# Optimization experiments

Measured on AMD Instinct MI355X. Metric: run time of the kernel, lower is better.

The kernel has to match this reference:

```python
import jax, jax.numpy as jnp
import numpy as np

B, T, C = 4, 2048, 1024
H = 16
D = C // H  # head_dim = 64

def setup_inputs() -> dict:
    key = jax.random.key(0)
    k1, k2, k3 = jax.random.split(key, 3)
    x = jax.random.normal(k1, (B, T, C), dtype=jnp.float32)
    Wqkv = jax.random.normal(k2, (C, 3 * C), dtype=jnp.float32) * (C ** -0.5)
    Wproj = jax.random.normal(k3, (C, C), dtype=jnp.float32) * (C ** -0.5)
    return {"x": x, "Wqkv": Wqkv, "Wproj": Wproj}

def reference(x, Wqkv, Wproj):
    b, t, c = x.shape
    qkv = (x @ Wqkv).reshape(b, t, 3, H, D)
    qkv = jnp.transpose(qkv, (2, 0, 3, 1, 4))  # [3, B, H, T, D]
    q, k, v = qkv[0], qkv[1], qkv[2]
    att = jnp.einsum('bhqd,bhkd->bhqk', q, k) * (D ** -0.5)
    causal = jnp.tril(jnp.ones((t, t), dtype=bool))  # True where allowed
    att = jnp.where(causal, att, -jnp.inf)
    att = jax.nn.softmax(att, axis=-1)
    out = jnp.einsum('bhqk,bhkd->bhqd', att, v)  # [B, H, T, D]
    out = jnp.transpose(out, (0, 2, 1, 3)).reshape(b, t, c)
    return out @ Wproj
```

## Files before the change

### kernel.cpp

```cpp
#include <hip/hip_runtime.h>
#include <stdint.h>

typedef unsigned short u16;
typedef __bf16 bf16x8 __attribute__((ext_vector_type(8)));
typedef float f32x4 __attribute__((ext_vector_type(4)));

#define DEVI static __device__ __forceinline__

DEVI u16 f2bf(float f) {
  union { float f; unsigned u; } v; v.f = f;
  unsigned r = v.u + 0x7FFF + ((v.u >> 16) & 1);
  return (u16)(r >> 16);
}

DEVI unsigned pkbf(float a, float b) {
  union { float f; unsigned u; } x, y; x.f = a; y.f = b;
  return __builtin_amdgcn_perm(y.u + 0x8000u, x.u + 0x8000u, 0x07060302u);
}

DEVI void lds_fence() { asm volatile("s_waitcnt lgkmcnt(0)" ::: "memory"); }

DEVI void gl2lds16(const u16* g, u16* l) {
  __builtin_amdgcn_global_load_lds(
      (const __attribute__((address_space(1))) unsigned int*)(uintptr_t)g,
      (__attribute__((address_space(3))) unsigned int*)(uintptr_t)l,
      16, 0, 0);
}

__global__ __launch_bounds__(256)
void prep(const float* __restrict__ x, u16* __restrict__ xb,
          const float* __restrict__ Wqkv, u16* __restrict__ wqkvT,
          const float* __restrict__ Wproj, u16* __restrict__ wprojT) {
  __shared__ float tile[64][65];
  const int blk = blockIdx.x;
  if (blk < 8192) {
    const int i = blk * 256 + threadIdx.x;
    const float4 v = ((const float4*)x)[i];
    ushort4 o;
    o.x = f2bf(v.x); o.y = f2bf(v.y); o.z = f2bf(v.z); o.w = f2bf(v.w);
    ((ushort4*)xb)[i] = o;
    return;
  }
  const float* in; u16* out; int Cn, n0, r0;
  if (blk < 8960) {
    const int p = blk - 8192;
    in = Wqkv; out = wqkvT; Cn = 3072;
    n0 = (p % 48) * 64; r0 = (p / 48) * 64;
  } else {
    const int p = blk - 8960;
    in = Wproj; out = wprojT; Cn = 1024;
    n0 = (p % 16) * 64; r0 = (p / 16) * 64;
  }
#pragma unroll
  for (int i = 0; i < 16; ++i) {
    const int e = threadIdx.x + i * 256;
    const int r = e >> 6, c = e & 63;
    tile[r][c] = in[(size_t)(r0 + r) * Cn + n0 + c];
  }
  __syncthreads();
#pragma unroll
  for (int i = 0; i < 16; ++i) {
    const int e = threadIdx.x + i * 256;
    const int r = e >> 6, c = e & 63;
    out[(size_t)(n0 + r) * 1024 + r0 + c] = f2bf(tile[c][r]);
  }
}

template <int MODE>
__global__ __launch_bounds__(256)
void gemm128(const u16* __restrict__ A, const u16* __restrict__ Bt,
             int M, int N, int K, float* __restrict__ Cout,
             u16* __restrict__ Qg, u16* __restrict__ Kg, u16* __restrict__ Vtg) {
  __shared__ alignas(16) u16 As0[128 * 32];
  __shared__ alignas(16) u16 As1[128 * 32];
  __shared__ alignas(16) u16 Bs0[128 * 32];
  __shared__ alignas(16) u16 Bs1[128 * 32];
  const int tid = threadIdx.x;
  const int wave = tid >> 6, lane = tid & 63;
  const int quad = lane >> 4, l15 = lane & 15;
  const int m0 = blockIdx.y * 128;
  const int n0 = blockIdx.x * 128;
  const int wm = (wave >> 1) * 64;
  const int wn = (wave & 1) * 64;

  f32x4 acc[4][4] = {};

  const int q1 = wave * 64 + lane;
  const int q2 = q1 + 256;
  const int r1 = q1 >> 2, c1 = q1 & 3;
  const int r2 = q2 >> 2, c2 = q2 & 3;
  const size_t ga1 = (size_t)(m0 + r1) * K + c1 * 8;
  const size_t ga2 = (size_t)(m0 + r2) * K + c2 * 8;
  const size_t gb1 = (size_t)(n0 + r1) * K + c1 * 8;
  const size_t gb2 = (size_t)(n0 + r2) * K + c2 * 8;

  for (int k0 = 0; k0 < K; k0 += 64) {
    __syncthreads();
    gl2lds16(A + ga1 + k0, As0 + wave * 512);
    gl2lds16(A + ga2 + k0, As0 + 2048 + wave * 512);
    gl2lds16(Bt + gb1 + k0, Bs0 + wave * 512);
    gl2lds16(Bt + gb2 + k0, Bs0 + 2048 + wave * 512);
    gl2lds16(A + ga1 + k0 + 32, As1 + wave * 512);
    gl2lds16(A + ga2 + k0 + 32, As1 + 2048 + wave * 512);
    gl2lds16(Bt + gb1 + k0 + 32, Bs1 + wave * 512);
    gl2lds16(Bt + gb2 + k0 + 32, Bs1 + 2048 + wave * 512);
    __syncthreads();
#pragma unroll
    for (int kh = 0; kh < 2; ++kh) {
      const u16* Asl = kh ? As1 : As0;
      const u16* Bsl = kh ? Bs1 : Bs0;
      bf16x8 av[4], bv[4];
#pragma unroll
      for (int i = 0; i < 4; ++i)
        av[i] = *(const bf16x8*)(Asl + (wm + i * 16 + l15) * 32 + quad * 8);
#pragma unroll
      for (int j = 0; j < 4; ++j)
        bv[j] = *(const bf16x8*)(Bsl + (wn + j * 16 + l15) * 32 + quad * 8);
#pragma unroll
      for (int i = 0; i < 4; ++i)
#pragma unroll
        for (int j = 0; j < 4; ++j)
          acc[i][j] = __builtin_amdgcn_mfma_f32_16x16x32_bf16(av[i], bv[j], acc[i][j], 0, 0, 0);
    }
  }

  if constexpr (MODE == 0) {
#pragma unroll
    for (int i = 0; i < 4; ++i) {
#pragma unroll
      for (int j = 0; j < 4; ++j) {
        const int mb = m0 + wm + i * 16 + quad * 4;
        const int n = n0 + wn + j * 16 + l15;
#pragma unroll
        for (int r = 0; r < 4; ++r)
          Cout[(size_t)(mb + r) * N + n] = acc[i][j][r];
      }
    }
  } else {
    const int s0b = n0 >> 10;
    const int b = m0 >> 11;
    const int h = ((n0 + wn) >> 6) & 15;
    const int bh = b * 16 + h;
    const int tbase = (m0 & 2047) + wm;
    if (s0b == 2) {
      __syncthreads();
      u16* sl = (wave < 2 ? As0 : Bs0) + (wave & 1) * 2048;
#pragma unroll
      for (int jp = 0; jp < 2; ++jp) {
#pragma unroll
        for (int j2 = 0; j2 < 2; ++j2) {
          const int j = jp * 2 + j2;
          const int dl = j2 * 16 + l15;
          const int sw8 = dl & 7;
#pragma unroll
          for (int i = 0; i < 4; ++i) {
            const int tq = i * 2 + (quad >> 1);
            ushort4 pk;
            pk.x = f2bf(acc[i][j][0]); pk.y = f2bf(acc[i][j][1]);
            pk.z = f2bf(acc[i][j][2]); pk.w = f2bf(acc[i][j][3]);
            *(ushort4*)(sl + dl * 64 + ((tq ^ sw8) << 3) + (quad & 1) * 4) = pk;
          }
        }
        lds_fence();
#pragma unroll
        for (int p = 0; p < 4; ++p) {
          const int dl = p * 8 + (lane >> 3);
          const int tc = lane & 7;
          const int tcu = tc ^ (dl & 7);
          const uint4 v = *(const uint4*)(sl + dl * 64 + tc * 8);
          *(uint4*)(Vtg + ((size_t)(bh * 64 + jp * 32 + dl)) * 2048 + tbase + tcu * 8) = v;
        }
        lds_fence();
      }
    } else {
      u16* dst = s0b ? Kg : Qg;
      const float scale = s0b ? 1.0f : 0.18033688f;
#pragma unroll
      for (int i = 0; i < 4; ++i) {
        const int t0 = tbase + i * 16 + quad * 4;
#pragma unroll
        for (int j = 0; j < 4; ++j) {
          const int d = j * 16 + l15;
#pragma unroll
          for (int r = 0; r < 4; ++r)
            dst[((size_t)bh * 2048 + t0 + r) * 64 + d] = f2bf(acc[i][j][r] * scale);
        }
      }
    }
  }
}

__global__ __launch_bounds__(256)
void attn_fwd(const u16* __restrict__ Qg, const u16* __restrict__ Kg,
              const u16* __restrict__ Vtg, u16* __restrict__ Og) {
  __shared__ alignas(16) u16 Ks[2][64 * 64];
  __shared__ alignas(16) u16 Vts[2][64 * 64];
  __shared__ alignas(16) u16 Ps[4][16 * 64];

  const int tid = threadIdx.x;
  const int wave = tid >> 6, lane = tid & 63;
  const int quad = lane >> 4, l15 = lane & 15;
  const int bh = blockIdx.x & 63;
  const int qt = 15 - (blockIdx.x >> 6);
  const int b = bh >> 4, h = bh & 15;
  const int sw = l15 & 7;

  const int rs0 = wave * 16 + (lane >> 3);
  const int rs1 = rs0 + 8;
  const int cs = (lane & 7) ^ (rs0 & 7);
  const size_t kgb0 = (size_t)(bh * 2048 + rs0) * 64 + cs * 8;
  const size_t kgb1 = (size_t)(bh * 2048 + rs1) * 64 + cs * 8;
  const size_t vgb0 = (size_t)(bh * 64 + rs0) * 2048 + cs * 8;
  const size_t vgb1 = (size_t)(bh * 64 + rs1) * 2048 + cs * 8;
  const int ldsw0 = wave * 1024;
  const int ldsw1 = wave * 1024 + 512;

  const int qb0 = qt * 128 + wave * 32;

  bf16x8 bq[2][2];
#pragma unroll
  for (int qs = 0; qs < 2; ++qs)
#pragma unroll
    for (int hv = 0; hv < 2; ++hv)
      bq[qs][hv] = *(const bf16x8*)(Qg + ((size_t)bh * 2048 + qb0 + qs * 16 + l15) * 64 + hv * 32 + quad * 8);

  f32x4 oacc[2][4] = {};
  float li[2] = {0.f, 0.f};

  const int jlast = qt * 128 + 64;
  const int nt = (jlast >> 6) + 1;

  gl2lds16(Kg + kgb0, Ks[0] + ldsw0);
  gl2lds16(Kg + kgb1, Ks[0] + ldsw1);
  gl2lds16(Vtg + vgb0, Vts[0] + ldsw0);
  gl2lds16(Vtg + vgb1, Vts[0] + ldsw1);
  asm volatile("s_waitcnt vmcnt(0)" ::: "memory");
  __builtin_amdgcn_s_barrier();

  for (int t = 0; t < nt; ++t) {
    const int j0 = t << 6;
    const int cur = t & 1;
    if (t + 1 < nt) {
      const size_t ko = (size_t)(j0 + 64) * 64;
      gl2lds16(Kg + kgb0 + ko, Ks[cur ^ 1] + ldsw0);
      gl2lds16(Kg + kgb1 + ko, Ks[cur ^ 1] + ldsw1);
      gl2lds16(Vtg + vgb0 + j0 + 64, Vts[cur ^ 1] + ldsw0);
      gl2lds16(Vtg + vgb1 + j0 + 64, Vts[cur ^ 1] + ldsw1);
    }

    if (j0 <= qb0 + 31) {
      __builtin_amdgcn_s_setprio(1);
      const u16* Kc = Ks[cur];
      const u16* Vc = Vts[cur];
      bf16x8 aK[4][2];
#pragma unroll
      for (int ks = 0; ks < 4; ++ks)
#pragma unroll
        for (int hv = 0; hv < 2; ++hv)
          aK[ks][hv] = *(const bf16x8*)(Kc + (ks * 16 + l15) * 64 + ((hv * 4 + quad) ^ sw) * 8);
      bf16x8 bV[4][2];
#pragma unroll
      for (int ds = 0; ds < 4; ++ds)
#pragma unroll
        for (int kc = 0; kc < 2; ++kc)
          bV[ds][kc] = *(const bf16x8*)(Vc + (ds * 16 + l15) * 64 + ((kc * 4 + quad) ^ sw) * 8);

#pragma unroll
      for (int qs = 0; qs < 2; ++qs) {
        const int qb = qb0 + qs * 16;
        if (j0 > qb + 15) continue;
        u16* Pw = Ps[wave];
        const bool needmask = (j0 + 63 > qb);
#pragma unroll
        for (int ks = 0; ks < 4; ++ks) {
          f32x4 s = {};
          s = __builtin_amdgcn_mfma_f32_16x16x32_bf16(aK[ks][0], bq[qs][0], s, 0, 0, 0);
          s = __builtin_amdgcn_mfma_f32_16x16x32_bf16(aK[ks][1], bq[qs][1], s, 0, 0, 0);
          if (needmask) {
            const int kbase = j0 + ks * 16 + quad * 4;
            const int qrow = qb + l15;
#pragma unroll
            for (int r = 0; r < 4; ++r)
              if (kbase + r > qrow) s[r] = -1e30f;
          }
          float p0 = __builtin_amdgcn_exp2f(s[0]);
          float p1 = __builtin_amdgcn_exp2f(s[1]);
          float p2 = __builtin_amdgcn_exp2f(s[2]);
          float p3 = __builtin_amdgcn_exp2f(s[3]);
          li[qs] += (p0 + p1) + (p2 + p3);
          uint2 pk;
          pk.x = pkbf(p0, p1);
          pk.y = pkbf(p2, p3);
          *(uint2*)(Pw + l15 * 64 + (((ks * 2 + (quad >> 1)) ^ sw) * 8) + (quad & 1) * 4) = pk;
        }
        lds_fence();
        bf16x8 aP0 = *(const bf16x8*)(Pw + l15 * 64 + ((0 * 4 + quad) ^ sw) * 8);
        bf16x8 aP1 = *(const bf16x8*)(Pw + l15 * 64 + ((1 * 4 + quad) ^ sw) * 8);
#pragma unroll
        for (int ds = 0; ds < 4; ++ds) {
          oacc[qs][ds] = __builtin_amdgcn_mfma_f32_16x16x32_bf16(aP0, bV[ds][0], oacc[qs][ds], 0, 0, 0);
          oacc[qs][ds] = __builtin_amdgcn_mfma_f32_16x16x32_bf16(aP1, bV[ds][1], oacc[qs][ds], 0, 0, 0);
        }
      }
      __builtin_amdgcn_s_setprio(0);
    }

    asm volatile("s_waitcnt vmcnt(0)" ::: "memory");
    __builtin_amdgcn_s_barrier();
  }

#pragma unroll
  for (int qs = 0; qs < 2; ++qs) {
    float l = li[qs];
    l += __shfl_xor(l, 16);
    l += __shfl_xor(l, 32);
    const int qb = qb0 + qs * 16;
#pragma unroll
    for (int r = 0; r < 4; ++r) {
      const float lrow = __shfl(l, quad * 4 + r);
      const float inv = 1.0f / lrow;
      u16* orow = Og + ((size_t)b * 2048 + qb + quad * 4 + r) * 1024 + h * 64;
#pragma unroll
      for (int ds = 0; ds < 4; ++ds)
        orow[ds * 16 + l15] = f2bf(oacc[qs][ds][r] * inv);
    }
  }
}

extern "C" void kernel_launch(void* const* d_in, const int* in_sizes, int n_in,
                              void* d_out, int out_size, void* d_ws, size_t ws_size,
                              hipStream_t stream) {
  const float* x = (const float*)d_in[0];
  const float* Wqkv = (const float*)d_in[1];
  const float* Wproj = (const float*)d_in[2];
  float* out = (float*)d_out;

  char* ws = (char*)d_ws;
  u16* xb     = (u16*)(ws);
  u16* wqkvT  = (u16*)(ws + 16777216);
  u16* wprojT = (u16*)(ws + 23068672);
  u16* Qg     = (u16*)(ws + 25165824);
  u16* Kg     = (u16*)(ws + 41943040);
  u16* Vtg    = (u16*)(ws + 58720256);
  u16* Og     = (u16*)(ws + 75497472);

  prep<<<9216, 256, 0, stream>>>(x, xb, Wqkv, wqkvT, Wproj, wprojT);
  gemm128<1><<<dim3(24, 64), 256, 0, stream>>>(xb, wqkvT, 8192, 3072, 1024,
                                               nullptr, Qg, Kg, Vtg);
  attn_fwd<<<1024, 256, 0, stream>>>(Qg, Kg, Vtg, Og);
  gemm128<0><<<dim3(8, 64), 256, 0, stream>>>(Og, wprojT, 8192, 1024, 1024,
                                              out, nullptr, nullptr, nullptr);
}
```

Before: 243.3 us.

## Pair complementary 64-row query tiles per block for causal load balance

```diff
diff --git a/kernel.cpp b/kernel.cpp
--- a/kernel.cpp
+++ b/kernel.cpp
@@ -201,7 +201,7 @@
   const int wave = tid >> 6, lane = tid & 63;
   const int quad = lane >> 4, l15 = lane & 15;
   const int bh = blockIdx.x & 63;
-  const int qt = 15 - (blockIdx.x >> 6);
+  const int ip = blockIdx.x >> 6;
   const int b = bh >> 4, h = bh & 15;
   const int sw = l15 & 7;
 
@@ -215,40 +215,35 @@
   const int ldsw0 = wave * 1024;
   const int ldsw1 = wave * 1024 + 512;
 
-  const int qb0 = qt * 128 + wave * 32;
-
-  bf16x8 bq[2][2];
-#pragma unroll
-  for (int qs = 0; qs < 2; ++qs)
-#pragma unroll
-    for (int hv = 0; hv < 2; ++hv)
-      bq[qs][hv] = *(const bf16x8*)(Qg + ((size_t)bh * 2048 + qb0 + qs * 16 + l15) * 64 + hv * 32 + quad * 8);
-
-  f32x4 oacc[2][4] = {};
-  float li[2] = {0.f, 0.f};
-
-  const int jlast = qt * 128 + 64;
-  const int nt = (jlast >> 6) + 1;
-
-  gl2lds16(Kg + kgb0, Ks[0] + ldsw0);
-  gl2lds16(Kg + kgb1, Ks[0] + ldsw1);
-  gl2lds16(Vtg + vgb0, Vts[0] + ldsw0);
-  gl2lds16(Vtg + vgb1, Vts[0] + ldsw1);
-  asm volatile("s_waitcnt vmcnt(0)" ::: "memory");
-  __builtin_amdgcn_s_barrier();
-
-  for (int t = 0; t < nt; ++t) {
-    const int j0 = t << 6;
-    const int cur = t & 1;
-    if (t + 1 < nt) {
-      const size_t ko = (size_t)(j0 + 64) * 64;
-      gl2lds16(Kg + kgb0 + ko, Ks[cur ^ 1] + ldsw0);
-      gl2lds16(Kg + kgb1 + ko, Ks[cur ^ 1] + ldsw1);
-      gl2lds16(Vtg + vgb0 + j0 + 64, Vts[cur ^ 1] + ldsw0);
-      gl2lds16(Vtg + vgb1 + j0 + 64, Vts[cur ^ 1] + ldsw1);
-    }
-
-    if (j0 <= qb0 + 31) {
+#pragma unroll 1
+  for (int ph = 0; ph < 2; ++ph) {
+    const int g = ph ? ip : (31 - ip);
+    const int qb = g * 64 + wave * 16;
+
+    const bf16x8 bq0 = *(const bf16x8*)(Qg + ((size_t)bh * 2048 + qb + l15) * 64 + quad * 8);
+    const bf16x8 bq1 = *(const bf16x8*)(Qg + ((size_t)bh * 2048 + qb + l15) * 64 + 32 + quad * 8);
+
+    f32x4 oacc[4] = {};
+    float li = 0.f;
+
+    gl2lds16(Kg + kgb0, Ks[0] + ldsw0);
+    gl2lds16(Kg + kgb1, Ks[0] + ldsw1);
+    gl2lds16(Vtg + vgb0, Vts[0] + ldsw0);
+    gl2lds16(Vtg + vgb1, Vts[0] + ldsw1);
+    asm volatile("s_waitcnt vmcnt(0)" ::: "memory");
+    __builtin_amdgcn_s_barrier();
+
+    for (int t = 0; t <= g; ++t) {
+      const int j0 = t << 6;
+      const int cur = t & 1;
+      if (t < g) {
+        const size_t ko = (size_t)(j0 + 64) * 64;
+        gl2lds16(Kg + kgb0 + ko, Ks[cur ^ 1] + ldsw0);
+        gl2lds16(Kg + kgb1 + ko, Ks[cur ^ 1] + ldsw1);
+        gl2lds16(Vtg + vgb0 + j0 + 64, Vts[cur ^ 1] + ldsw0);
+        gl2lds16(Vtg + vgb1 + j0 + 64, Vts[cur ^ 1] + ldsw1);
+      }
+
       __builtin_amdgcn_s_setprio(1);
       const u16* Kc = Ks[cur];
       const u16* Vc = Vts[cur];
@@ -265,56 +260,47 @@
         for (int kc = 0; kc < 2; ++kc)
           bV[ds][kc] = *(const bf16x8*)(Vc + (ds * 16 + l15) * 64 + ((kc * 4 + quad) ^ sw) * 8);
 
-#pragma unroll
-      for (int qs = 0; qs < 2; ++qs) {
-        const int qb = qb0 + qs * 16;
-        if (j0 > qb + 15) continue;
-        u16* Pw = Ps[wave];
-        const bool needmask = (j0 + 63 > qb);
-#pragma unroll
-        for (int ks = 0; ks < 4; ++ks) {
-          f32x4 s = {};
-          s = __builtin_amdgcn_mfma_f32_16x16x32_bf16(aK[ks][0], bq[qs][0], s, 0, 0, 0);
-          s = __builtin_amdgcn_mfma_f32_16x16x32_bf16(aK[ks][1], bq[qs][1], s, 0, 0, 0);
-          if (needmask) {
-            const int kbase = j0 + ks * 16 + quad * 4;
-            const int qrow = qb + l15;
-#pragma unroll
-            for (int r = 0; r < 4; ++r)
-              if (kbase + r > qrow) s[r] = -1e30f;
-          }
-          float p0 = __builtin_amdgcn_exp2f(s[0]);
-          float p1 = __builtin_amdgcn_exp2f(s[1]);
-          float p2 = __builtin_amdgcn_exp2f(s[2]);
-          float p3 = __builtin_amdgcn_exp2f(s[3]);
-          li[qs] += (p0 + p1) + (p2 + p3);
-          uint2 pk;
-          pk.x = pkbf(p0, p1);
-          pk.y = pkbf(p2, p3);
-          *(uint2*)(Pw + l15 * 64 + (((ks * 2 + (quad >> 1)) ^ sw) * 8) + (quad & 1) * 4) = pk;
+      u16* Pw = Ps[wave];
+      const bool needmask = (t == g);
+#pragma unroll
+      for (int ks = 0; ks < 4; ++ks) {
+        f32x4 s = {};
+        s = __builtin_amdgcn_mfma_f32_16x16x32_bf16(aK[ks][0], bq0, s, 0, 0, 0);
+        s = __builtin_amdgcn_mfma_f32_16x16x32_bf16(aK[ks][1], bq1, s, 0, 0, 0);
+        if (needmask) {
+          const int kbase = j0 + ks * 16 + quad * 4;
+          const int qrow = qb + l15;
+#pragma unroll
+          for (int r = 0; r < 4; ++r)
+            if (kbase + r > qrow) s[r] = -1e30f;
         }
-        lds_fence();
-        bf16x8 aP0 = *(const bf16x8*)(Pw + l15 * 64 + ((0 * 4 + quad) ^ sw) * 8);
-        bf16x8 aP1 = *(const bf16x8*)(Pw + l15 * 64 + ((1 * 4 + quad) ^ sw) * 8);
-#pragma unroll
-        for (int ds = 0; ds < 4; ++ds) {
-          oacc[qs][ds] = __builtin_amdgcn_mfma_f32_16x16x32_bf16(aP0, bV[ds][0], oacc[qs][ds], 0, 0, 0);
-          oacc[qs][ds] = __builtin_amdgcn_mfma_f32_16x16x32_bf16(aP1, bV[ds][1], oacc[qs][ds], 0, 0, 0);
-        }
+        float p0 = __builtin_amdgcn_exp2f(s[0]);
+        float p1 = __builtin_amdgcn_exp2f(s[1]);
+        float p2 = __builtin_amdgcn_exp2f(s[2]);
+        float p3 = __builtin_amdgcn_exp2f(s[3]);
+        li += (p0 + p1) + (p2 + p3);
+        uint2 pk;
+        pk.x = pkbf(p0, p1);
+        pk.y = pkbf(p2, p3);
+        *(uint2*)(Pw + l15 * 64 + (((ks * 2 + (quad >> 1)) ^ sw) * 8) + (quad & 1) * 4) = pk;
+      }
+      lds_fence();
+      bf16x8 aP0 = *(const bf16x8*)(Pw + l15 * 64 + ((0 * 4 + quad) ^ sw) * 8);
+      bf16x8 aP1 = *(const bf16x8*)(Pw + l15 * 64 + ((1 * 4 + quad) ^ sw) * 8);
+#pragma unroll
+      for (int ds = 0; ds < 4; ++ds) {
+        oacc[ds] = __builtin_amdgcn_mfma_f32_16x16x32_bf16(aP0, bV[ds][0], oacc[ds], 0, 0, 0);
+        oacc[ds] = __builtin_amdgcn_mfma_f32_16x16x32_bf16(aP1, bV[ds][1], oacc[ds], 0, 0, 0);
       }
       __builtin_amdgcn_s_setprio(0);
-    }
-
-    asm volatile("s_waitcnt vmcnt(0)" ::: "memory");
-    __builtin_amdgcn_s_barrier();
-  }
-
-#pragma unroll
-  for (int qs = 0; qs < 2; ++qs) {
-    float l = li[qs];
+
+      asm volatile("s_waitcnt vmcnt(0)" ::: "memory");
+      __builtin_amdgcn_s_barrier();
+    }
+
+    float l = li;
     l += __shfl_xor(l, 16);
     l += __shfl_xor(l, 32);
-    const int qb = qb0 + qs * 16;
 #pragma unroll
     for (int r = 0; r < 4; ++r) {
       const float lrow = __shfl(l, quad * 4 + r);
@@ -322,7 +308,7 @@
       u16* orow = Og + ((size_t)b * 2048 + qb + quad * 4 + r) * 1024 + h * 64;
 #pragma unroll
       for (int ds = 0; ds < 4; ++ds)
-        orow[ds * 16 + l15] = f2bf(oacc[qs][ds][r] * inv);
+        orow[ds * 16 + l15] = f2bf(oacc[ds][r] * inv);
     }
   }
 }
```

Result: slower. 254.6 us (+4.7%).
